# Optimization experiments

Hardware: AMD Instinct MI355X
Metric: run time of the kernel (lower is better)

The kernel has to match this reference:

```python
import jax, jax.numpy as jnp
import numpy as np

ALPHABET = 26

def _shift(position, S):
    if position == 0:
        return jnp.zeros(S, dtype=jnp.int32)
    elif position == 1:
        return jnp.arange(S, dtype=jnp.int32) % ALPHABET
    elif position == 2:
        return jnp.arange(S, dtype=jnp.int32) // 26 + 1 % 26  # faithful to torch precedence: +1
    elif position == 3:
        return jnp.arange(S, dtype=jnp.int32) // 676 + 1 % 26
    raise ValueError('Invalid rotor position')


def setup_inputs() -> dict:
    key = jax.random.key(0)
    k1, k2 = jax.random.split(key)
    B, S = 128, 8192
    signalInput = jax.random.normal(k1, (B, S, ALPHABET), dtype=jnp.float32)
    # xavier_normal_ on a 26x26 matrix: std = sqrt(2/(26+26))
    std = float(np.sqrt(2.0 / (ALPHABET + ALPHABET)))
    rotor = jax.random.normal(k2, (ALPHABET, ALPHABET), dtype=jnp.float32) * std
    return {"signalInput": signalInput, "rotor": rotor}


def reference(signalInput, rotor):
    position = 1
    B, S, _ = signalInput.shape
    # L2-normalize rotor rows (torch.norm(dim=1, keepdim=True))
    rn = rotor / jnp.linalg.norm(rotor, axis=1, keepdims=True)  # [26,26]
    shift = _shift(position, S)                                  # [S]
    # one_hot((i + shift[s]) % 26) @ rn  ==  gather rn rows
    idx = (jnp.arange(ALPHABET, dtype=jnp.int32)[None, :] + shift[:, None]) % ALPHABET  # [S,26]
    M = rn[idx]                                                  # [S,26,26]
    # per-token 1x26 @ 26x26 bmm, batch-independent rotation matrix
    out = jnp.einsum('bsi,sij->bsj', signalInput, M)             # [B,S,26]
    return jax.nn.softmax(out, axis=2)
```

## Files before the change

### kernel.cpp

```cpp
#include <hip/hip_runtime.h>
#include <math.h>

#define ALPHA 26
#define ROW_PAD 32
#define TPB 256

typedef __attribute__((address_space(3))) float lds_f;
typedef const __attribute__((address_space(1))) float glb_f;

__global__ void rotor_norm_kernel(const float* __restrict__ rotor,
                                  float* __restrict__ rn) {
    int i = threadIdx.x;
    if (i < ALPHA) {
        float ss = 0.f;
        #pragma unroll
        for (int j = 0; j < ALPHA; ++j) {
            float v = rotor[i * ALPHA + j];
            ss += v * v;
        }
        float inv = 1.0f / sqrtf(ss);
        #pragma unroll
        for (int j = 0; j < ALPHA; ++j)
            rn[i * ROW_PAD + j] = rotor[i * ALPHA + j] * inv;
    }
}

__global__ __launch_bounds__(TPB, 6) void rotor_main(
        const float* __restrict__ x,
        const float* __restrict__ rn,
        float* __restrict__ out) {
    __shared__ float tile[TPB * ALPHA];

    const int tid  = threadIdx.x;
    const int lane = tid & 63;
    const int wave = tid >> 6;

    const long long blockF = (long long)blockIdx.x * (TPB * ALPHA);
    const int waveF = wave * (64 * ALPHA);
    const float* gin  = x   + blockF;
    float*       gout = out + blockF;

    #pragma unroll
    for (int it = 0; it < 6; ++it) {
        __builtin_amdgcn_global_load_lds(
            (glb_f*)(gin + waveF + it * 256 + lane * 4),
            (lds_f*)&tile[waveF + it * 256],
            16, 0, 0);
    }
    {
        float2 d = *(const float2*)(gin + waveF + 1536 + lane * 2);
        *(float2*)&tile[waveF + 1536 + lane * 2] = d;
    }
    asm volatile("s_waitcnt vmcnt(0)" ::: "memory");

    const int n = blockIdx.x * TPB + tid;
    const int r = (n & 8191) % 26;
    int shift = 26 - r; if (shift == 26) shift = 0;

    const float* myx = &tile[tid * ALPHA];
    float xv[ALPHA];
    #pragma unroll
    for (int k = 0; k < ALPHA; ++k) {
        int idx = k + shift;
        idx = (idx >= ALPHA) ? idx - ALPHA : idx;
        xv[k] = myx[idx];
    }

    float acc[ALPHA];
    #pragma unroll
    for (int j = 0; j < ALPHA; ++j) acc[j] = 0.f;

    #pragma unroll
    for (int k = 0; k < ALPHA; ++k) {
        const float xk = xv[k];
        #pragma unroll
        for (int j = 0; j < ALPHA; ++j)
            acc[j] = fmaf(xk, rn[k * ROW_PAD + j], acc[j]);
    }

    float m = acc[0];
    #pragma unroll
    for (int j = 1; j < ALPHA; ++j) m = fmaxf(m, acc[j]);
    float sum = 0.f;
    #pragma unroll
    for (int j = 0; j < ALPHA; ++j) { acc[j] = __expf(acc[j] - m); sum += acc[j]; }
    float inv = 1.0f / sum;
    #pragma unroll
    for (int j = 0; j < ALPHA; ++j) acc[j] *= inv;

    #pragma unroll
    for (int j = 0; j < ALPHA; ++j)
        tile[tid * ALPHA + j] = acc[j];

    #pragma unroll
    for (int it = 0; it < 6; ++it) {
        float4 d = *(const float4*)&tile[waveF + it * 256 + lane * 4];
        *(float4*)(gout + waveF + it * 256 + lane * 4) = d;
    }
    {
        float2 d = *(const float2*)&tile[waveF + 1536 + lane * 2];
        *(float2*)(gout + waveF + 1536 + lane * 2) = d;
    }
}

extern "C" void kernel_launch(void* const* d_in, const int* in_sizes, int n_in,
                              void* d_out, int out_size, void* d_ws, size_t ws_size,
                              hipStream_t stream) {
    const float* x     = (const float*)d_in[0];
    const float* rotor = (const float*)d_in[1];
    float* out = (float*)d_out;
    float* rn  = (float*)d_ws;

    rotor_norm_kernel<<<1, 64, 0, stream>>>(rotor, rn);

    const int tokens = out_size / ALPHA;
    const int blocks = tokens / TPB;
    rotor_main<<<blocks, TPB, 0, stream>>>(x, rn, out);
}
```

Before: 203.0 us.

## Compute rotor matmul with bf16 MFMA instead of per-thread FMAs

Replaces the per-thread 26x26 scalar FMA loop with 16x16x32 bf16 MFMA instructions. The normalized rotor is stored as a padded bf16 matrix and held in registers as B fragments. Activations are rotated, converted to bf16 and fed as A fragments. Results are scattered through LDS for a row-wise softmax. This cuts VALU and rotor-load work, at the cost of bf16 precision on inputs and weights.

```diff
diff --git a/kernel.cpp b/kernel.cpp
--- a/kernel.cpp
+++ b/kernel.cpp
@@ -2,41 +2,66 @@
 #include <math.h>
 
 #define ALPHA 26
-#define ROW_PAD 32
 #define TPB 256
+#define ROWF 26
+#define WAVEF (64 * ROWF)
 
+typedef __attribute__((ext_vector_type(8))) short short8;
+typedef __attribute__((ext_vector_type(4))) float float4v;
 typedef __attribute__((address_space(3))) float lds_f;
 typedef const __attribute__((address_space(1))) float glb_f;
 
+__device__ __forceinline__ unsigned short f2bf(float f) {
+    unsigned u = __builtin_bit_cast(unsigned, f);
+    u += 0x7FFFu + ((u >> 16) & 1u);
+    return (unsigned short)(u >> 16);
+}
+
 __global__ void rotor_norm_kernel(const float* __restrict__ rotor,
-                                  float* __restrict__ rn) {
-    int i = threadIdx.x;
-    if (i < ALPHA) {
-        float ss = 0.f;
-        #pragma unroll
-        for (int j = 0; j < ALPHA; ++j) {
-            float v = rotor[i * ALPHA + j];
-            ss += v * v;
+                                  unsigned short* __restrict__ rnb) {
+    int k = threadIdx.x;
+    if (k < 32) {
+        if (k < ALPHA) {
+            float ss = 0.f;
+            #pragma unroll
+            for (int j = 0; j < ALPHA; ++j) {
+                float v = rotor[k * ALPHA + j];
+                ss += v * v;
+            }
+            float inv = 1.0f / sqrtf(ss);
+            #pragma unroll
+            for (int n = 0; n < 32; ++n)
+                rnb[k * 32 + n] = (n < ALPHA) ? f2bf(rotor[k * ALPHA + n] * inv)
+                                              : (unsigned short)0;
+        } else {
+            #pragma unroll
+            for (int n = 0; n < 32; ++n) rnb[k * 32 + n] = 0;
         }
-        float inv = 1.0f / sqrtf(ss);
-        #pragma unroll
-        for (int j = 0; j < ALPHA; ++j)
-            rn[i * ROW_PAD + j] = rotor[i * ALPHA + j] * inv;
     }
 }
 
 __global__ __launch_bounds__(TPB, 6) void rotor_main(
         const float* __restrict__ x,
-        const float* __restrict__ rn,
+        const unsigned short* __restrict__ rnb,
         float* __restrict__ out) {
-    __shared__ float tile[TPB * ALPHA];
+    __shared__ float stage[4 * WAVEF];
 
     const int tid  = threadIdx.x;
     const int lane = tid & 63;
     const int wave = tid >> 6;
+    const int n15  = lane & 15;
+    const int quad = lane >> 4;
+    const int waveF = wave * WAVEF;
+
+    short8 bfrag0, bfrag1;
+    #pragma unroll
+    for (int j = 0; j < 8; ++j) {
+        int k = quad * 8 + j;
+        bfrag0[j] = (short)rnb[k * 32 + n15];
+        bfrag1[j] = (short)rnb[k * 32 + 16 + n15];
+    }
 
     const long long blockF = (long long)blockIdx.x * (TPB * ALPHA);
-    const int waveF = wave * (64 * ALPHA);
     const float* gin  = x   + blockF;
     float*       gout = out + blockF;
 
@@ -44,61 +69,77 @@
     for (int it = 0; it < 6; ++it) {
         __builtin_amdgcn_global_load_lds(
             (glb_f*)(gin + waveF + it * 256 + lane * 4),
-            (lds_f*)&tile[waveF + it * 256],
+            (lds_f*)&stage[waveF + it * 256],
             16, 0, 0);
     }
     {
         float2 d = *(const float2*)(gin + waveF + 1536 + lane * 2);
-        *(float2*)&tile[waveF + 1536 + lane * 2] = d;
+        *(float2*)&stage[waveF + 1536 + lane * 2] = d;
     }
     asm volatile("s_waitcnt vmcnt(0)" ::: "memory");
 
-    const int n = blockIdx.x * TPB + tid;
-    const int r = (n & 8191) % 26;
-    int shift = 26 - r; if (shift == 26) shift = 0;
-
-    const float* myx = &tile[tid * ALPHA];
-    float xv[ALPHA];
+    const int tokBase = blockIdx.x * TPB + wave * 64;
+    float4v accA[4], accB[4];
     #pragma unroll
-    for (int k = 0; k < ALPHA; ++k) {
-        int idx = k + shift;
-        idx = (idx >= ALPHA) ? idx - ALPHA : idx;
-        xv[k] = myx[idx];
+    for (int m = 0; m < 4; ++m) {
+        accA[m] = (float4v){0.f, 0.f, 0.f, 0.f};
+        accB[m] = (float4v){0.f, 0.f, 0.f, 0.f};
     }
 
-    float acc[ALPHA];
     #pragma unroll
-    for (int j = 0; j < ALPHA; ++j) acc[j] = 0.f;
+    for (int m = 0; m < 4; ++m) {
+        const int tok = tokBase + m * 16 + n15;
+        const int r = (tok & 8191) % 26;
+        const int rowOff = waveF + (m * 16 + n15) * ROWF;
+        const int k0 = quad * 8;
+        int idx0 = k0 - r; if (idx0 < 0) idx0 += 26;
+
+        short8 af;
+        #pragma unroll
+        for (int j = 0; j < 8; ++j) {
+            int idx = idx0 + j; if (idx >= 26) idx -= 26;
+            float v = stage[rowOff + idx];
+            v = (k0 + j < ALPHA) ? v : 0.f;
+            af[j] = (short)f2bf(v);
+        }
+        accA[m] = __builtin_amdgcn_mfma_f32_16x16x32_bf16(af, bfrag0, accA[m], 0, 0, 0);
+        accB[m] = __builtin_amdgcn_mfma_f32_16x16x32_bf16(af, bfrag1, accB[m], 0, 0, 0);
+    }
 
     #pragma unroll
-    for (int k = 0; k < ALPHA; ++k) {
-        const float xk = xv[k];
+    for (int m = 0; m < 4; ++m) {
         #pragma unroll
-        for (int j = 0; j < ALPHA; ++j)
-            acc[j] = fmaf(xk, rn[k * ROW_PAD + j], acc[j]);
+        for (int rg = 0; rg < 4; ++rg) {
+            const int base = waveF + (m * 16 + quad * 4 + rg) * ROWF;
+            stage[base + n15] = accA[m][rg];
+            if (n15 < ALPHA - 16)
+                stage[base + 16 + n15] = accB[m][rg];
+        }
     }
+    asm volatile("s_waitcnt lgkmcnt(0)" ::: "memory");
 
-    float m = acc[0];
+    const float* myrow = &stage[waveF + lane * ROWF];
+    float v[ALPHA];
     #pragma unroll
-    for (int j = 1; j < ALPHA; ++j) m = fmaxf(m, acc[j]);
+    for (int j = 0; j < ALPHA; ++j) v[j] = myrow[j];
+    float mx = v[0];
+    #pragma unroll
+    for (int j = 1; j < ALPHA; ++j) mx = fmaxf(mx, v[j]);
     float sum = 0.f;
     #pragma unroll
-    for (int j = 0; j < ALPHA; ++j) { acc[j] = __expf(acc[j] - m); sum += acc[j]; }
+    for (int j = 0; j < ALPHA; ++j) { v[j] = __expf(v[j] - mx); sum += v[j]; }
     float inv = 1.0f / sum;
+    float* wrow = &stage[waveF + lane * ROWF];
     #pragma unroll
-    for (int j = 0; j < ALPHA; ++j) acc[j] *= inv;
-
-    #pragma unroll
-    for (int j = 0; j < ALPHA; ++j)
-        tile[tid * ALPHA + j] = acc[j];
+    for (int j = 0; j < ALPHA; ++j) wrow[j] = v[j] * inv;
 
     #pragma unroll
     for (int it = 0; it < 6; ++it) {
-        float4 d = *(const float4*)&tile[waveF + it * 256 + lane * 4];
+        float4 d = *(const float4*)&stage[waveF + it * 256 + lane * 4];
         *(float4*)(gout + waveF + it * 256 + lane * 4) = d;
     }
     {
-        float2 d = *(const float2*)&tile[waveF + 1536 + lane * 2];
+        float2 d = *(const float2*)&stage[waveF + 1536 + lane * 2];
         *(float2*)(gout + waveF + 1536 + lane * 2) = d;
     }
 }
@@ -109,11 +150,11 @@
     const float* x     = (const float*)d_in[0];
     const float* rotor = (const float*)d_in[1];
     float* out = (float*)d_out;
-    float* rn  = (float*)d_ws;
+    unsigned short* rnb = (unsigned short*)d_ws;
 
-    rotor_norm_kernel<<<1, 64, 0, stream>>>(rotor, rn);
+    rotor_norm_kernel<<<1, 64, 0, stream>>>(rotor, rnb);
 
     const int tokens = out_size / ALPHA;
     const int blocks = tokens / TPB;
-    rotor_main<<<blocks, TPB, 0, stream>>>(x, rn, out);
+    rotor_main<<<blocks, TPB, 0, stream>>>(x, rnb, out);
 }
```

Measured after the change: 194.2 us. 1.04x faster.
